# Kernel optimization log

Measured on AMD Instinct MI355X. Metric: run time of the kernel, lower is better.

The kernel has to match this reference:

```python
import jax, jax.numpy as jnp
import numpy as np


def setup_inputs() -> dict:
    key = jax.random.key(0)
    ks = jax.random.split(key, 16)
    B, S, H = 512, 128, 256
    f32 = jnp.float32
    inputs = jax.random.normal(ks[0], (B, S, 2), f32)
    # xavier-normal-ish init (gain/sqrt(fan_in+fan_out) approximated by small scale)
    def xn(k, shape):
        fan = shape[0] + shape[1]
        return jax.random.normal(k, shape, f32) * np.sqrt(2.0 / fan)
    return {
        "inputs": inputs,
        "W0": xn(ks[1], (H, 2)),   "b0": jnp.zeros((H,), f32),
        "W1": xn(ks[2], (H, H)),   "b1": jnp.zeros((H,), f32),
        "W2": xn(ks[3], (H, H)),   "b2": jnp.zeros((H,), f32),
        "W3": xn(ks[4], (H, H)),   "b3": jnp.zeros((H,), f32),
        "W4": xn(ks[5], (1, H)),   "b4": jnp.zeros((1,), f32),
        "log_growth_rate": jax.random.normal(ks[6], (), f32),
        "log_carrying_capacity": jax.random.normal(ks[7], (), f32),
        "log_initial_loss": jax.random.normal(ks[8], (), f32),
        "in_mean": jnp.array([0.5, 50.0], f32),
        "in_std": jnp.array([0.2, 30.0], f32),
        "tgt_mean": jnp.array([0.8], f32),
        "tgt_std": jnp.array([0.1], f32),
    }


def reference(inputs, W0, b0, W1, b1, W2, b2, W3, b3, W4, b4,
              log_growth_rate, log_carrying_capacity, log_initial_loss,
              in_mean, in_std, tgt_mean, tgt_std):
    B, S = inputs.shape[0], inputs.shape[1]
    # PDE parameters (Verhulst logistic growth)
    r = jnp.exp(-log_growth_rate)
    K = 0.2 + (1.0 - 0.2) * jax.nn.sigmoid(log_carrying_capacity)  # carrying capacity in [0.2, 1]
    C = 0.0 + (0.1 - 0.0) * jax.nn.sigmoid(log_initial_loss)       # initial loss in [0, 0.1]

    # split state feature s and time t, standardize per-column
    s = inputs[..., 0:1].reshape(-1, 1)  # [N,1]
    t = inputs[..., 1:2].reshape(-1, 1)  # [N,1]
    s_norm = (s - in_mean[0:1]) / (in_std[0:1] + 1e-8)
    t_norm = (t - in_mean[1:2]) / (in_std[1:2] + 1e-8)

    Ws = (W0, W1, W2, W3, W4)
    bs = (b0, b1, b2, b3, b4)

    def mlp(x):  # [N,2] -> [N,1], tanh MLP
        h = x
        for W, b in zip(Ws[:-1], bs[:-1]):
            h = jnp.tanh(h @ W.T + b)
        return h @ Ws[-1].T + bs[-1]

    def u_of(tn):  # U(s_norm, tn), inverse-standardized targets
        return mlp(jnp.concatenate([s_norm, tn], axis=-1)) * tgt_std + tgt_mean

    ones = jnp.ones_like(t_norm)

    def uf_of(tn):
        # U and U_t = dU/dt_norm (forward-mode; each point depends on its own scalar t)
        U, U_dot = jax.jvp(u_of, (tn,), (ones,))
        U_t = U_dot.sum(-1, keepdims=True)
        G = r * (U - C) * (1.0 - (U - C) / (K - C))  # Verhulst
        return U, U_t - G  # (U, F)

    # second derivative w.r.t. t_norm: F_t = U_tt - G_t
    (U, F), (_, F_t) = jax.jvp(uf_of, (t_norm,), (ones,))

    shp = (B, S, 1)
    return U.reshape(shp), F.reshape(shp), F_t.reshape(shp)
```

## Files before the change

kernel.cpp:

```cpp
#include <hip/hip_runtime.h>
#include <hip/hip_bf16.h>
#include <math.h>

typedef short s8v __attribute__((ext_vector_type(8)));
typedef float f4v __attribute__((ext_vector_type(4)));

#define HH 256
#define TP 32
#define NTHREADS 256
#define KSTR 520
#define TSTR 4160
#define NTILES 6
#define PLANE (NTILES * TSTR)

__device__ __forceinline__ unsigned short bf_rne(float x){
    union{float f;unsigned u;}v; v.f=x;
    unsigned r = v.u + 0x7FFFu + ((v.u >> 16) & 1u);
    return (unsigned short)(r >> 16);
}
__device__ __forceinline__ unsigned pack_rne2(float a, float b){
    union { __hip_bfloat162 h; unsigned u; } v;
    v.h = __float22bfloat162_rn(float2{a, b});
    return v.u;
}

__global__ __launch_bounds__(256)
void prep_weights(const float* __restrict__ W1, const float* __restrict__ W2,
                  const float* __restrict__ W3, const float* __restrict__ W0,
                  const float* __restrict__ b0, const float* __restrict__ W4,
                  unsigned short* __restrict__ wsB, float* __restrict__ wsF)
{
    int t = blockIdx.x * 256 + threadIdx.x;
    if (t < 24576) {
        int layer = t >> 13;
        int rem = t & 8191;
        int l  = rem & 63;
        int ks = (rem >> 6) & 7;
        int nt = rem >> 9;
        const float* W = (layer == 0) ? W1 : (layer == 1) ? W2 : W3;
        int n_out = nt * 16 + (l & 15);
        int quad  = l >> 4;
        const float* row = W + n_out * HH;
        s8v hi;
        #pragma unroll
        for (int j = 0; j < 8; ++j) {
            int n_in = quad * 64 + (j & 3) * 16 + ((j >> 2) << 3) + ks;
            hi[j] = (short)bf_rne(row[n_in]);
        }
        int dst = ((nt * 8 + ks) * 64 + l) * 8;
        *(s8v*)(wsB + layer * 65536 + dst) = hi;
    } else if (t < 24832) {
        int n = t - 24576;
        int pos = ((n & 7) * 4 + (n >> 6)) * 8 + ((n >> 4) & 3) + 4 * ((n >> 3) & 1);
        wsF[pos]       = W0[2 * n];
        wsF[256 + pos] = W0[2 * n + 1];
        wsF[512 + pos] = b0[n];
        wsF[768 + pos] = W4[n];
    }
}

__global__ __launch_bounds__(NTHREADS, 3)
void capnn_mfma(const float* __restrict__ inp,
                const float* __restrict__ b1, const float* __restrict__ b2,
                const float* __restrict__ b3, const float* __restrict__ b4,
                const float* __restrict__ W4raw,
                const float* __restrict__ lgr, const float* __restrict__ lcc,
                const float* __restrict__ lil,
                const float* __restrict__ imean, const float* __restrict__ istd,
                const float* __restrict__ tmean, const float* __restrict__ tstd,
                const unsigned short* __restrict__ wsW,
                const float* __restrict__ wsF,
                float* __restrict__ out, int N)
{
    __shared__ __align__(16) unsigned short Ahi[PLANE];
    __shared__ float sn_sh[TP], tn_sh[TP];
    __shared__ float head_part[TP * 3 * 4];

    const int tid  = threadIdx.x;
    const int lane = tid & 63;
    const int w    = tid >> 6;
    const int m16  = lane & 15;
    const int q    = lane >> 4;
    const int pbase = blockIdx.x * TP;

    const float* __restrict__ w00p = wsF;
    const float* __restrict__ w01p = wsF + 256;
    const float* __restrict__ b0p  = wsF + 512;

    float w4v[4];
    #pragma unroll
    for (int i = 0; i < 4; ++i) w4v[i] = W4raw[w * 64 + i * 16 + m16];

    if (tid < TP) {
        int pg = pbase + tid;
        float s = 0.f, t = 0.f;
        if (pg < N) { s = inp[2 * pg]; t = inp[2 * pg + 1]; }
        sn_sh[tid] = (s - imean[0]) / (istd[0] + 1e-8f);
        tn_sh[tid] = (t - imean[1]) / (istd[1] + 1e-8f);
    }
    __syncthreads();

    {
        const int l  = tid & 63;
        const int wv = tid >> 6;
        const int p16 = l & 15, quad = l >> 4;
        #pragma unroll
        for (int g2 = 0; g2 < 2; ++g2) {
            const int ks = wv + 4 * g2;
            const int pos = (ks * 4 + quad) * 8;
            float4 wA0 = *(const float4*)(w00p + pos);
            float4 wA1 = *(const float4*)(w00p + pos + 4);
            float4 wB0 = *(const float4*)(w01p + pos);
            float4 wB1 = *(const float4*)(w01p + pos + 4);
            float4 bb0 = *(const float4*)(b0p + pos);
            float4 bb1 = *(const float4*)(b0p + pos + 4);
            float w00v[8] = {wA0.x,wA0.y,wA0.z,wA0.w,wA1.x,wA1.y,wA1.z,wA1.w};
            float w01v[8] = {wB0.x,wB0.y,wB0.z,wB0.w,wB1.x,wB1.y,wB1.z,wB1.w};
            float b0v[8]  = {bb0.x,bb0.y,bb0.z,bb0.w,bb1.x,bb1.y,bb1.z,bb1.w};
            const int base = ks * KSTR + l * 8;
            #pragma unroll
            for (int h = 0; h < 2; ++h) {
                const float sn = sn_sh[h * 16 + p16], tn = tn_sh[h * 16 + p16];
                float av[8], d1v[8], d2v[8];
                #pragma unroll
                for (int j = 0; j < 8; ++j) {
                    float z = fmaf(w00v[j], sn, fmaf(w01v[j], tn, b0v[j]));
                    float e = __expf(2.f * z);
                    float a = 1.f - 2.f * __builtin_amdgcn_rcpf(e + 1.f);
                    float g = 1.f - a * a;
                    float d1 = g * w01v[j];
                    float d2 = -2.f * a * d1 * w01v[j];
                    av[j] = a; d1v[j] = d1; d2v[j] = d2;
                }
                #pragma unroll
                for (int s = 0; s < 3; ++s) {
                    const float* V = (s == 0) ? av : (s == 1) ? d1v : d2v;
                    int4 hi4;
                    hi4.x = (int)pack_rne2(V[0], V[1]);
                    hi4.y = (int)pack_rne2(V[2], V[3]);
                    hi4.z = (int)pack_rne2(V[4], V[5]);
                    hi4.w = (int)pack_rne2(V[6], V[7]);
                    *(int4*)&Ahi[(s * 2 + h) * TSTR + base] = hi4;
                }
            }
        }
    }
    __syncthreads();

    for (int L = 0; L < 3; ++L) {
        const unsigned short* __restrict__ Wlh = wsW + L * 65536;
        const float* __restrict__ bL = (L == 0) ? b1 : (L == 1) ? b2 : b3;

        f4v acc[NTILES][4];
        #pragma unroll
        for (int i = 0; i < 4; ++i) {
            float bias = bL[w * 64 + i * 16 + m16];
            acc[0][i] = (f4v){bias, bias, bias, bias};
            acc[1][i] = (f4v){bias, bias, bias, bias};
            #pragma unroll
            for (int t = 2; t < NTILES; ++t)
                acc[t][i] = (f4v){0.f, 0.f, 0.f, 0.f};
        }

        #pragma unroll
        for (int ks = 0; ks < 8; ++ks) {
            s8v ah[NTILES];
            const int aoff = ks * KSTR + lane * 8;
            #pragma unroll
            for (int t = 0; t < NTILES; ++t)
                ah[t] = *(const s8v*)&Ahi[t * TSTR + aoff];
            #pragma unroll
            for (int i = 0; i < 4; ++i) {
                const int off = (((w * 4 + i) * 8 + ks) * 64 + lane) * 8;
                s8v bh = *(const s8v*)(Wlh + off);
                #pragma unroll
                for (int t = 0; t < NTILES; ++t)
                    acc[t][i] = __builtin_amdgcn_mfma_f32_16x16x32_bf16(ah[t], bh, acc[t][i], 0, 0, 0);
            }
        }

        if (L < 2) {
            __syncthreads();
            const int ksw  = m16 & 7;
            const int hsel = m16 >> 3;
            const int wbase = ksw * KSTR + (16 * w + q * 4) * 8 + 4 * hsel;
            #pragma unroll
            for (int h = 0; h < 2; ++h) {
                #pragma unroll
                for (int r = 0; r < 4; ++r) {
                    float Av[3][4];
                    #pragma unroll
                    for (int i = 0; i < 4; ++i) {
                        float z  = acc[h][i][r];
                        float z1 = acc[2 + h][i][r];
                        float z2 = acc[4 + h][i][r];
                        float e = __expf(2.f * z);
                        float a = 1.f - 2.f * __builtin_amdgcn_rcpf(e + 1.f);
                        float g = 1.f - a * a;
                        float d1 = g * z1;
                        float d2 = fmaf(g, z2, -2.f * a * d1 * z1);
                        Av[0][i] = a; Av[1][i] = d1; Av[2][i] = d2;
                    }
                    #pragma unroll
                    for (int s = 0; s < 3; ++s) {
                        int2 hi2;
                        hi2.x = (int)pack_rne2(Av[s][0], Av[s][1]);
                        hi2.y = (int)pack_rne2(Av[s][2], Av[s][3]);
                        *(int2*)&Ahi[(s * 2 + h) * TSTR + wbase + r * 8] = hi2;
                    }
                }
            }
            __syncthreads();
        } else {
            float hp[3][2][4];
            #pragma unroll
            for (int s = 0; s < 3; ++s)
                #pragma unroll
                for (int h = 0; h < 2; ++h)
                    #pragma unroll
                    for (int r = 0; r < 4; ++r) hp[s][h][r] = 0.f;
            #pragma unroll
            for (int h = 0; h < 2; ++h) {
                #pragma unroll
                for (int r = 0; r < 4; ++r) {
                    #pragma unroll
                    for (int i = 0; i < 4; ++i) {
                        float z  = acc[h][i][r];
                        float z1 = acc[2 + h][i][r];
                        float z2 = acc[4 + h][i][r];
                        float e = __expf(2.f * z);
                        float a = 1.f - 2.f * __builtin_amdgcn_rcpf(e + 1.f);
                        float g = 1.f - a * a;
                        float d1 = g * z1;
                        float d2 = fmaf(g, z2, -2.f * a * d1 * z1);
                        hp[0][h][r] = fmaf(w4v[i], a,  hp[0][h][r]);
                        hp[1][h][r] = fmaf(w4v[i], d1, hp[1][h][r]);
                        hp[2][h][r] = fmaf(w4v[i], d2, hp[2][h][r]);
                    }
                }
            }
            #pragma unroll
            for (int m = 1; m < 16; m <<= 1) {
                #pragma unroll
                for (int s = 0; s < 3; ++s)
                    #pragma unroll
                    for (int h = 0; h < 2; ++h)
                        #pragma unroll
                        for (int r = 0; r < 4; ++r)
                            hp[s][h][r] += __shfl_xor(hp[s][h][r], m);
            }
            if (m16 == 0) {
                #pragma unroll
                for (int s = 0; s < 3; ++s)
                    #pragma unroll
                    for (int h = 0; h < 2; ++h)
                        #pragma unroll
                        for (int r = 0; r < 4; ++r)
                            head_part[(s * TP + h * 16 + q * 4 + r) * 4 + w] = hp[s][h][r];
            }
            __syncthreads();
        }
    }

    if (tid < TP) {
        float sv = 0.f, s1v = 0.f, s2v = 0.f;
        #pragma unroll
        for (int ww = 0; ww < 4; ++ww) {
            sv  += head_part[(0 * TP + tid) * 4 + ww];
            s1v += head_part[(1 * TP + tid) * 4 + ww];
            s2v += head_part[(2 * TP + tid) * 4 + ww];
        }
        int pg = pbase + tid;
        if (pg < N) {
            float r_  = expf(-lgr[0]);
            float Kc  = 0.2f + 0.8f / (1.f + expf(-lcc[0]));
            float Cc  = 0.1f / (1.f + expf(-lil[0]));
            float kci = 1.f / (Kc - Cc);
            float ts = tstd[0], tm = tmean[0];
            float U   = (sv + b4[0]) * ts + tm;
            float Ut  = s1v * ts;
            float Utt = s2v * ts;
            float Um  = U - Cc;
            float G   = r_ * Um * (1.f - Um * kci);
            float Gt  = r_ * Ut * (1.f - 2.f * Um * kci);
            out[pg]         = U;
            out[N + pg]     = Ut - G;
            out[2 * N + pg] = Utt - Gt;
        }
    }
}

extern "C" void kernel_launch(void* const* d_in, const int* in_sizes, int n_in,
                              void* d_out, int out_size, void* d_ws, size_t ws_size,
                              hipStream_t stream) {
    const float* inp   = (const float*)d_in[0];
    const float* W0    = (const float*)d_in[1];
    const float* b0    = (const float*)d_in[2];
    const float* W1    = (const float*)d_in[3];
    const float* b1    = (const float*)d_in[4];
    const float* W2    = (const float*)d_in[5];
    const float* b2    = (const float*)d_in[6];
    const float* W3    = (const float*)d_in[7];
    const float* b3    = (const float*)d_in[8];
    const float* W4    = (const float*)d_in[9];
    const float* b4    = (const float*)d_in[10];
    const float* lgr   = (const float*)d_in[11];
    const float* lcc   = (const float*)d_in[12];
    const float* lil   = (const float*)d_in[13];
    const float* imean = (const float*)d_in[14];
    const float* istd  = (const float*)d_in[15];
    const float* tmean = (const float*)d_in[16];
    const float* tstd  = (const float*)d_in[17];

    unsigned short* wsB = (unsigned short*)d_ws;
    float* wsF = (float*)((char*)d_ws + 393216);

    const int N = in_sizes[0] / 2;
    const int gridMain = (N + TP - 1) / TP;

    hipLaunchKernelGGL(prep_weights, dim3(97), dim3(256), 0, stream,
                       W1, W2, W3, W0, b0, W4, wsB, wsF);
    hipLaunchKernelGGL(capnn_mfma, dim3(gridMain), dim3(NTHREADS), 0, stream,
                       inp, b1, b2, b3, b4, W4,
                       lgr, lcc, lil, imean, istd, tmean, tstd,
                       wsB, wsF, (float*)d_out, N);
}
```

Measured before the change: 177.9 us.

## Ping-pong two 16-point halves to overlap MFMA with tanh epilogues

Splits each block's 32 points into two 16-point halves with separate accumulator sets. The MFMA k-loop of one half is interleaved with the tanh/derivative epilogue (and layer-0 setup and head reduction) of the other half, so matrix and vector ALU work can overlap instead of running in serial phases. Biases are hoisted into registers up front. Launch bounds drop from 3 to 2 blocks per CU to give room for the extra live registers, which reduces occupancy.

After: 185.7 us. 4.4% more time.

```diff
diff --git a/kernel.cpp b/kernel.cpp
--- a/kernel.cpp
+++ b/kernel.cpp
@@ -59,7 +59,7 @@
     }
 }
 
-__global__ __launch_bounds__(NTHREADS, 3)
+__global__ __launch_bounds__(NTHREADS, 2)
 void capnn_mfma(const float* __restrict__ inp,
                 const float* __restrict__ b1, const float* __restrict__ b2,
                 const float* __restrict__ b3, const float* __restrict__ b4,
@@ -87,9 +87,15 @@
     const float* __restrict__ w01p = wsF + 256;
     const float* __restrict__ b0p  = wsF + 512;
 
-    float w4v[4];
-    #pragma unroll
-    for (int i = 0; i < 4; ++i) w4v[i] = W4raw[w * 64 + i * 16 + m16];
+    float w4v[4], biasv[3][4];
+    #pragma unroll
+    for (int i = 0; i < 4; ++i) {
+        const int n = w * 64 + i * 16 + m16;
+        w4v[i] = W4raw[n];
+        biasv[0][i] = b1[n];
+        biasv[1][i] = b2[n];
+        biasv[2][i] = b3[n];
+    }
 
     if (tid < TP) {
         int pg = pbase + tid;
@@ -100,167 +106,205 @@
     }
     __syncthreads();
 
-    {
+    auto l0_half = [&](int h, int g2) {
         const int l  = tid & 63;
         const int wv = tid >> 6;
         const int p16 = l & 15, quad = l >> 4;
-        #pragma unroll
-        for (int g2 = 0; g2 < 2; ++g2) {
-            const int ks = wv + 4 * g2;
-            const int pos = (ks * 4 + quad) * 8;
-            float4 wA0 = *(const float4*)(w00p + pos);
-            float4 wA1 = *(const float4*)(w00p + pos + 4);
-            float4 wB0 = *(const float4*)(w01p + pos);
-            float4 wB1 = *(const float4*)(w01p + pos + 4);
-            float4 bb0 = *(const float4*)(b0p + pos);
-            float4 bb1 = *(const float4*)(b0p + pos + 4);
-            float w00v[8] = {wA0.x,wA0.y,wA0.z,wA0.w,wA1.x,wA1.y,wA1.z,wA1.w};
-            float w01v[8] = {wB0.x,wB0.y,wB0.z,wB0.w,wB1.x,wB1.y,wB1.z,wB1.w};
-            float b0v[8]  = {bb0.x,bb0.y,bb0.z,bb0.w,bb1.x,bb1.y,bb1.z,bb1.w};
-            const int base = ks * KSTR + l * 8;
+        const int ks = wv + 4 * g2;
+        const int pos = (ks * 4 + quad) * 8;
+        float4 wA0 = *(const float4*)(w00p + pos);
+        float4 wA1 = *(const float4*)(w00p + pos + 4);
+        float4 wB0 = *(const float4*)(w01p + pos);
+        float4 wB1 = *(const float4*)(w01p + pos + 4);
+        float4 bb0 = *(const float4*)(b0p + pos);
+        float4 bb1 = *(const float4*)(b0p + pos + 4);
+        float w00v[8] = {wA0.x,wA0.y,wA0.z,wA0.w,wA1.x,wA1.y,wA1.z,wA1.w};
+        float w01v[8] = {wB0.x,wB0.y,wB0.z,wB0.w,wB1.x,wB1.y,wB1.z,wB1.w};
+        float b0v[8]  = {bb0.x,bb0.y,bb0.z,bb0.w,bb1.x,bb1.y,bb1.z,bb1.w};
+        const float sn = sn_sh[h * 16 + p16], tn = tn_sh[h * 16 + p16];
+        float av[8], d1v[8], d2v[8];
+        #pragma unroll
+        for (int j = 0; j < 8; ++j) {
+            float z = fmaf(w00v[j], sn, fmaf(w01v[j], tn, b0v[j]));
+            float e = __expf(2.f * z);
+            float a = 1.f - 2.f * __builtin_amdgcn_rcpf(e + 1.f);
+            float g = 1.f - a * a;
+            float d1 = g * w01v[j];
+            float d2 = -2.f * a * d1 * w01v[j];
+            av[j] = a; d1v[j] = d1; d2v[j] = d2;
+        }
+        const int base = ks * KSTR + l * 8;
+        #pragma unroll
+        for (int s = 0; s < 3; ++s) {
+            const float* V = (s == 0) ? av : (s == 1) ? d1v : d2v;
+            int4 hi4;
+            hi4.x = (int)pack_rne2(V[0], V[1]);
+            hi4.y = (int)pack_rne2(V[2], V[3]);
+            hi4.z = (int)pack_rne2(V[4], V[5]);
+            hi4.w = (int)pack_rne2(V[6], V[7]);
+            *(int4*)&Ahi[(s * 2 + h) * TSTR + base] = hi4;
+        }
+    };
+
+    auto kstep = [&](int h, f4v (&acc)[3][4], const unsigned short* __restrict__ Wl, int ks) {
+        s8v a[3];
+        const int aoff = ks * KSTR + lane * 8;
+        #pragma unroll
+        for (int s = 0; s < 3; ++s)
+            a[s] = *(const s8v*)&Ahi[(s * 2 + h) * TSTR + aoff];
+        #pragma unroll
+        for (int i = 0; i < 4; ++i) {
+            const int off = (((w * 4 + i) * 8 + ks) * 64 + lane) * 8;
+            s8v bh = *(const s8v*)(Wl + off);
             #pragma unroll
-            for (int h = 0; h < 2; ++h) {
-                const float sn = sn_sh[h * 16 + p16], tn = tn_sh[h * 16 + p16];
-                float av[8], d1v[8], d2v[8];
-                #pragma unroll
-                for (int j = 0; j < 8; ++j) {
-                    float z = fmaf(w00v[j], sn, fmaf(w01v[j], tn, b0v[j]));
-                    float e = __expf(2.f * z);
-                    float a = 1.f - 2.f * __builtin_amdgcn_rcpf(e + 1.f);
-                    float g = 1.f - a * a;
-                    float d1 = g * w01v[j];
-                    float d2 = -2.f * a * d1 * w01v[j];
-                    av[j] = a; d1v[j] = d1; d2v[j] = d2;
-                }
-                #pragma unroll
-                for (int s = 0; s < 3; ++s) {
-                    const float* V = (s == 0) ? av : (s == 1) ? d1v : d2v;
-                    int4 hi4;
-                    hi4.x = (int)pack_rne2(V[0], V[1]);
-                    hi4.y = (int)pack_rne2(V[2], V[3]);
-                    hi4.z = (int)pack_rne2(V[4], V[5]);
-                    hi4.w = (int)pack_rne2(V[6], V[7]);
-                    *(int4*)&Ahi[(s * 2 + h) * TSTR + base] = hi4;
-                }
-            }
-        }
-    }
-    __syncthreads();
-
-    for (int L = 0; L < 3; ++L) {
-        const unsigned short* __restrict__ Wlh = wsW + L * 65536;
-        const float* __restrict__ bL = (L == 0) ? b1 : (L == 1) ? b2 : b3;
-
-        f4v acc[NTILES][4];
+            for (int s = 0; s < 3; ++s)
+                acc[s][i] = __builtin_amdgcn_mfma_f32_16x16x32_bf16(a[s], bh, acc[s][i], 0, 0, 0);
+        }
+    };
+
+    auto initacc = [&](f4v (&acc)[3][4], int L) {
         #pragma unroll
         for (int i = 0; i < 4; ++i) {
-            float bias = bL[w * 64 + i * 16 + m16];
-            acc[0][i] = (f4v){bias, bias, bias, bias};
-            acc[1][i] = (f4v){bias, bias, bias, bias};
-            #pragma unroll
-            for (int t = 2; t < NTILES; ++t)
-                acc[t][i] = (f4v){0.f, 0.f, 0.f, 0.f};
-        }
-
-        #pragma unroll
-        for (int ks = 0; ks < 8; ++ks) {
-            s8v ah[NTILES];
-            const int aoff = ks * KSTR + lane * 8;
-            #pragma unroll
-            for (int t = 0; t < NTILES; ++t)
-                ah[t] = *(const s8v*)&Ahi[t * TSTR + aoff];
-            #pragma unroll
-            for (int i = 0; i < 4; ++i) {
-                const int off = (((w * 4 + i) * 8 + ks) * 64 + lane) * 8;
-                s8v bh = *(const s8v*)(Wlh + off);
-                #pragma unroll
-                for (int t = 0; t < NTILES; ++t)
-                    acc[t][i] = __builtin_amdgcn_mfma_f32_16x16x32_bf16(ah[t], bh, acc[t][i], 0, 0, 0);
-            }
-        }
-
-        if (L < 2) {
-            __syncthreads();
-            const int ksw  = m16 & 7;
-            const int hsel = m16 >> 3;
-            const int wbase = ksw * KSTR + (16 * w + q * 4) * 8 + 4 * hsel;
-            #pragma unroll
-            for (int h = 0; h < 2; ++h) {
-                #pragma unroll
-                for (int r = 0; r < 4; ++r) {
-                    float Av[3][4];
-                    #pragma unroll
-                    for (int i = 0; i < 4; ++i) {
-                        float z  = acc[h][i][r];
-                        float z1 = acc[2 + h][i][r];
-                        float z2 = acc[4 + h][i][r];
-                        float e = __expf(2.f * z);
-                        float a = 1.f - 2.f * __builtin_amdgcn_rcpf(e + 1.f);
-                        float g = 1.f - a * a;
-                        float d1 = g * z1;
-                        float d2 = fmaf(g, z2, -2.f * a * d1 * z1);
-                        Av[0][i] = a; Av[1][i] = d1; Av[2][i] = d2;
-                    }
-                    #pragma unroll
-                    for (int s = 0; s < 3; ++s) {
-                        int2 hi2;
-                        hi2.x = (int)pack_rne2(Av[s][0], Av[s][1]);
-                        hi2.y = (int)pack_rne2(Av[s][2], Av[s][3]);
-                        *(int2*)&Ahi[(s * 2 + h) * TSTR + wbase + r * 8] = hi2;
-                    }
-                }
-            }
-            __syncthreads();
-        } else {
-            float hp[3][2][4];
+            float b = biasv[L][i];
+            acc[0][i] = (f4v){b, b, b, b};
+            acc[1][i] = (f4v){0.f, 0.f, 0.f, 0.f};
+            acc[2][i] = (f4v){0.f, 0.f, 0.f, 0.f};
+        }
+    };
+
+    auto tchunk = [&](int h, int r, const f4v (&acc)[3][4]) {
+        const int ksw  = m16 & 7;
+        const int hsel = m16 >> 3;
+        const int wbase = ksw * KSTR + (16 * w + q * 4) * 8 + 4 * hsel;
+        float Av[3][4];
+        #pragma unroll
+        for (int i = 0; i < 4; ++i) {
+            float z  = acc[0][i][r];
+            float z1 = acc[1][i][r];
+            float z2 = acc[2][i][r];
+            float e = __expf(2.f * z);
+            float a = 1.f - 2.f * __builtin_amdgcn_rcpf(e + 1.f);
+            float g = 1.f - a * a;
+            float d1 = g * z1;
+            float d2 = fmaf(g, z2, -2.f * a * d1 * z1);
+            Av[0][i] = a; Av[1][i] = d1; Av[2][i] = d2;
+        }
+        #pragma unroll
+        for (int s = 0; s < 3; ++s) {
+            int2 hi2;
+            hi2.x = (int)pack_rne2(Av[s][0], Av[s][1]);
+            hi2.y = (int)pack_rne2(Av[s][2], Av[s][3]);
+            *(int2*)&Ahi[(s * 2 + h) * TSTR + wbase + r * 8] = hi2;
+        }
+    };
+
+    auto headchunk = [&](int r, const f4v (&acc)[3][4], float (&hp)[3][4]) {
+        #pragma unroll
+        for (int i = 0; i < 4; ++i) {
+            float z  = acc[0][i][r];
+            float z1 = acc[1][i][r];
+            float z2 = acc[2][i][r];
+            float e = __expf(2.f * z);
+            float a = 1.f - 2.f * __builtin_amdgcn_rcpf(e + 1.f);
+            float g = 1.f - a * a;
+            float d1 = g * z1;
+            float d2 = fmaf(g, z2, -2.f * a * d1 * z1);
+            hp[0][r] = fmaf(w4v[i], a,  hp[0][r]);
+            hp[1][r] = fmaf(w4v[i], d1, hp[1][r]);
+            hp[2][r] = fmaf(w4v[i], d2, hp[2][r]);
+        }
+    };
+
+    auto headflush = [&](int h, float (&hp)[3][4]) {
+        #pragma unroll
+        for (int m = 1; m < 16; m <<= 1)
             #pragma unroll
             for (int s = 0; s < 3; ++s)
                 #pragma unroll
-                for (int h = 0; h < 2; ++h)
-                    #pragma unroll
-                    for (int r = 0; r < 4; ++r) hp[s][h][r] = 0.f;
+                for (int r = 0; r < 4; ++r)
+                    hp[s][r] += __shfl_xor(hp[s][r], m);
+        if (m16 == 0) {
             #pragma unroll
-            for (int h = 0; h < 2; ++h) {
+            for (int s = 0; s < 3; ++s)
                 #pragma unroll
-                for (int r = 0; r < 4; ++r) {
-                    #pragma unroll
-                    for (int i = 0; i < 4; ++i) {
-                        float z  = acc[h][i][r];
-                        float z1 = acc[2 + h][i][r];
-                        float z2 = acc[4 + h][i][r];
-                        float e = __expf(2.f * z);
-                        float a = 1.f - 2.f * __builtin_amdgcn_rcpf(e + 1.f);
-                        float g = 1.f - a * a;
-                        float d1 = g * z1;
-                        float d2 = fmaf(g, z2, -2.f * a * d1 * z1);
-                        hp[0][h][r] = fmaf(w4v[i], a,  hp[0][h][r]);
-                        hp[1][h][r] = fmaf(w4v[i], d1, hp[1][h][r]);
-                        hp[2][h][r] = fmaf(w4v[i], d2, hp[2][h][r]);
-                    }
-                }
-            }
-            #pragma unroll
-            for (int m = 1; m < 16; m <<= 1) {
-                #pragma unroll
-                for (int s = 0; s < 3; ++s)
-                    #pragma unroll
-                    for (int h = 0; h < 2; ++h)
-                        #pragma unroll
-                        for (int r = 0; r < 4; ++r)
-                            hp[s][h][r] += __shfl_xor(hp[s][h][r], m);
-            }
-            if (m16 == 0) {
-                #pragma unroll
-                for (int s = 0; s < 3; ++s)
-                    #pragma unroll
-                    for (int h = 0; h < 2; ++h)
-                        #pragma unroll
-                        for (int r = 0; r < 4; ++r)
-                            head_part[(s * TP + h * 16 + q * 4 + r) * 4 + w] = hp[s][h][r];
-            }
-            __syncthreads();
-        }
-    }
+                for (int r = 0; r < 4; ++r)
+                    head_part[(s * TP + h * 16 + q * 4 + r) * 4 + w] = hp[s][r];
+        }
+    };
+
+    const unsigned short* __restrict__ W1p = wsW;
+    const unsigned short* __restrict__ W2p = wsW + 65536;
+    const unsigned short* __restrict__ W3p = wsW + 131072;
+
+    f4v accA[3][4], accB[3][4];
+
+    l0_half(0, 0);
+    l0_half(0, 1);
+    __syncthreads();
+
+    initacc(accA, 0);
+    #pragma unroll
+    for (int ks = 0; ks < 8; ++ks) {
+        kstep(0, accA, W1p, ks);
+        if (ks == 1) l0_half(1, 0);
+        if (ks == 4) l0_half(1, 1);
+    }
+    __syncthreads();
+
+    initacc(accB, 0);
+    #pragma unroll
+    for (int ks = 0; ks < 8; ++ks) {
+        kstep(1, accB, W1p, ks);
+        if (ks & 1) tchunk(0, ks >> 1, accA);
+    }
+    __syncthreads();
+
+    initacc(accA, 1);
+    #pragma unroll
+    for (int ks = 0; ks < 8; ++ks) {
+        kstep(0, accA, W2p, ks);
+        if (ks & 1) tchunk(1, ks >> 1, accB);
+    }
+    __syncthreads();
+
+    initacc(accB, 1);
+    #pragma unroll
+    for (int ks = 0; ks < 8; ++ks) {
+        kstep(1, accB, W2p, ks);
+        if (ks & 1) tchunk(0, ks >> 1, accA);
+    }
+    __syncthreads();
+
+    initacc(accA, 2);
+    #pragma unroll
+    for (int ks = 0; ks < 8; ++ks) {
+        kstep(0, accA, W3p, ks);
+        if (ks & 1) tchunk(1, ks >> 1, accB);
+    }
+    __syncthreads();
+
+    initacc(accB, 2);
+    float hp0[3][4];
+    #pragma unroll
+    for (int s = 0; s < 3; ++s)
+        #pragma unroll
+        for (int r = 0; r < 4; ++r) hp0[s][r] = 0.f;
+    #pragma unroll
+    for (int ks = 0; ks < 8; ++ks) {
+        kstep(1, accB, W3p, ks);
+        if (ks & 1) headchunk(ks >> 1, accA, hp0);
+    }
+    headflush(0, hp0);
+
+    float hp1[3][4];
+    #pragma unroll
+    for (int s = 0; s < 3; ++s)
+        #pragma unroll
+        for (int r = 0; r < 4; ++r) hp1[s][r] = 0.f;
+    #pragma unroll
+    for (int r = 0; r < 4; ++r) headchunk(r, accB, hp1);
+    headflush(1, hp1);
+    __syncthreads();
 
     if (tid < TP) {
         float sv = 0.f, s1v = 0.f, s2v = 0.f;
```
